# Optimization experiments

Measured on AMD Instinct MI355X. Metric: run time of the kernel, lower is better.

Reference implementation:

```python
import jax, jax.numpy as jnp
import numpy as np
import math

HIDDEN = 1024
HEADS = 16
HEAD = HIDDEN // HEADS
B, N = 2, 2048
NEG_INF = -10000.0


def setup_inputs() -> dict:
    key = jax.random.key(0)
    k1, k2, k3, k4, k5 = jax.random.split(key, 5)
    s = 1.0 / math.sqrt(HIDDEN)
    return {
        "encodings": jax.random.normal(k1, (B, N, HIDDEN), dtype=jnp.float32),
        "attn_w": jax.random.uniform(k2, (3 * HIDDEN, HIDDEN), minval=-s, maxval=s, dtype=jnp.float32),
        "attn_b": jax.random.uniform(k3, (3 * HIDDEN,), minval=-s, maxval=s, dtype=jnp.float32),
        "out_w": jax.random.uniform(k4, (HIDDEN, HIDDEN), minval=-s, maxval=s, dtype=jnp.float32),
        "out_b": jax.random.uniform(k5, (HIDDEN,), minval=-s, maxval=s, dtype=jnp.float32),
    }


def reference(encodings, attn_w, attn_b, out_w, out_b):
    b, n, _ = encodings.shape
    qkv = encodings @ attn_w.T + attn_b                      # [b, n, 3*hidden]
    # 'b n (h l) -> b h n l' with l = 3*head_size
    qkv = qkv.reshape(b, n, HEADS, 3 * HEAD).transpose(0, 2, 1, 3)  # [b, h, n, 3d]
    q, k, v = jnp.split(qkv, 3, axis=-1)                     # each [b, h, n, d]
    # causal mask: key index k attends only if k <= q
    mask = jnp.arange(n)[:, None] <= jnp.arange(n)[None, :]  # [k, q]
    scores = jnp.einsum('bhki,bhqi->bhkq', k, q) / math.sqrt(HEAD)
    scores = jnp.where(mask, scores, NEG_INF)
    probs = jax.nn.softmax(scores, axis=2)                   # softmax over k
    combined = jnp.einsum('bhkq,bhkl->bhql', probs, v)       # [b, h, n, d]
    out = combined.transpose(0, 2, 1, 3).reshape(b, n, HIDDEN)
    return out @ out_w.T + out_b
```

## Files before the change

kernel.cpp:

```cpp
#include <hip/hip_runtime.h>
#include <hip/hip_bf16.h>
#include <stdint.h>

#define HIDDEN 1024
#define NHEADS 16
#define DHEAD  64
#define BATCH  2
#define SEQ    2048
#define MROWS  (BATCH*SEQ)
#define QKVC   (3*HIDDEN)

typedef unsigned short u16;
typedef unsigned int   u32;
typedef __bf16 bf16x8 __attribute__((ext_vector_type(8)));
typedef __bf16 bf16x2 __attribute__((ext_vector_type(2)));
typedef float  f32x4  __attribute__((ext_vector_type(4)));
typedef float  f32x16 __attribute__((ext_vector_type(16)));
typedef short  s16x4  __attribute__((ext_vector_type(4)));
typedef u16    u16x8  __attribute__((ext_vector_type(8)));
typedef u32    u32x2  __attribute__((ext_vector_type(2)));

typedef const __attribute__((address_space(1))) void gvoid_t;
typedef       __attribute__((address_space(3))) void lvoid_t;

__device__ __forceinline__ gvoid_t* to_glob(const void* p){
  return (gvoid_t*)(uintptr_t)p;
}
__device__ __forceinline__ lvoid_t* to_lds(void* p){
  return (lvoid_t*)(uintptr_t)p;
}
__device__ __forceinline__ u32 lds_off(const void* p){
  return (u32)(uintptr_t)p;
}

__device__ __forceinline__ u16 f2bf(float x){
  __bf16 h = (__bf16)x;
  return __builtin_bit_cast(u16, h);
}
__device__ __forceinline__ u32 pk2(float a, float b){
  bf16x2 t = { (__bf16)a, (__bf16)b };
  return __builtin_bit_cast(u32, t);
}

#define MFMA32(a, b, c) __builtin_amdgcn_mfma_f32_32x32x16_bf16(a, b, c, 0, 0, 0)

__global__ __launch_bounds__(256) void k_cvt(const float* __restrict__ in,
                                             u16* __restrict__ out, int n4){
  int i = blockIdx.x * 256 + threadIdx.x;
  if (i >= n4) return;
  const float4 v = reinterpret_cast<const float4*>(in)[i];
  ushort4 o;
  o.x = f2bf(v.x); o.y = f2bf(v.y); o.z = f2bf(v.z); o.w = f2bf(v.w);
  reinterpret_cast<ushort4*>(out)[i] = o;
}

template<int NC, bool BF16OUT>
__global__ __launch_bounds__(256) void k_gemm(const u16* __restrict__ A,
                                              const u16* __restrict__ B,
                                              const float* __restrict__ bias,
                                              void* __restrict__ C){
  constexpr int K = HIDDEN;
  __shared__ u16 As[2][128*32];
  __shared__ u16 Bs[2][128*32];
  const int m0 = blockIdx.x * 128;
  const int n0 = blockIdx.y * 128;
  const int tid = threadIdx.x;
  const int w = tid >> 6, l = tid & 63;
  const int wr = w >> 1, wc = w & 1;

  const f32x4 fz = {0.f, 0.f, 0.f, 0.f};
  f32x4 acc[4][4];
  #pragma unroll
  for (int i = 0; i < 4; ++i)
    #pragma unroll
    for (int j = 0; j < 4; ++j) acc[i][j] = fz;

  const u16* ap = A + (size_t)(m0 + (tid >> 2)) * K + (tid & 3) * 8;
  const u16* bp = B + (size_t)(n0 + (tid >> 2)) * K + (tid & 3) * 8;

  auto stage = [&](int k0, int buf){
    __builtin_amdgcn_global_load_lds(to_glob(ap + k0),        to_lds(&As[buf][w*512]),        16, 0, 0);
    __builtin_amdgcn_global_load_lds(to_glob(ap + 64*K + k0), to_lds(&As[buf][2048 + w*512]), 16, 0, 0);
    __builtin_amdgcn_global_load_lds(to_glob(bp + k0),        to_lds(&Bs[buf][w*512]),        16, 0, 0);
    __builtin_amdgcn_global_load_lds(to_glob(bp + 64*K + k0), to_lds(&Bs[buf][2048 + w*512]), 16, 0, 0);
  };

  stage(0, 0);
  __syncthreads();

  for (int k0 = 0; k0 < K; k0 += 32){
    const int cur = (k0 >> 5) & 1;
    if (k0 + 32 < K) stage(k0 + 32, cur ^ 1);

    bf16x8 af[4], bfr[4];
    #pragma unroll
    for (int mf = 0; mf < 4; ++mf)
      af[mf]  = *(const bf16x8*)&As[cur][(wr*64 + mf*16 + (l & 15))*32 + (l >> 4)*8];
    #pragma unroll
    for (int nf = 0; nf < 4; ++nf)
      bfr[nf] = *(const bf16x8*)&Bs[cur][(wc*64 + nf*16 + (l & 15))*32 + (l >> 4)*8];
    #pragma unroll
    for (int mf = 0; mf < 4; ++mf)
      #pragma unroll
      for (int nf = 0; nf < 4; ++nf)
        acc[mf][nf] = __builtin_amdgcn_mfma_f32_16x16x32_bf16(af[mf], bfr[nf], acc[mf][nf], 0, 0, 0);

    __syncthreads();
  }

  #pragma unroll
  for (int nf = 0; nf < 4; ++nf){
    const int col = n0 + wc*64 + nf*16 + (l & 15);
    const float bv = bias[col];
    #pragma unroll
    for (int mf = 0; mf < 4; ++mf){
      #pragma unroll
      for (int r = 0; r < 4; ++r){
        const int row = m0 + wr*64 + mf*16 + (l >> 4)*4 + r;
        const float v = acc[mf][nf][r] + bv;
        if constexpr (BF16OUT) ((u16*)C)[(size_t)row * NC + col] = f2bf(v);
        else                   ((float*)C)[(size_t)row * NC + col] = v;
      }
    }
  }
}

__global__ __launch_bounds__(256) void k_attn(const u16* __restrict__ qkv,
                                              u16* __restrict__ aout){
  __shared__ u16 smem[2*16384];

  const int bh = blockIdx.x;
  const int b  = bh >> 4;
  const int h  = bh & 15;
  const int qt = 31 - blockIdx.y;
  const int tid = threadIdx.x;
  const int l  = tid & 63;
  const int w  = tid >> 6;
  const int hr = w >> 1;
  const int wr = w & 1;
  const int t128 = tid & 127;
  const int lw = t128 >> 6;
  const int nk = qt + 1;
  const int n0 = nk >> 1;
  const int myn = hr ? (nk - n0) : n0;
  const int kb  = hr ? n0 : 0;
  const int trips = nk - n0;
  const int q0 = qt*64 + wr*32;
  const size_t base = (size_t)b * SEQ * QKVC + (size_t)h * 192;
  const float CEXP = 0.18033688011112042f;

  u16* const Kreg = smem + hr*16384;
  u16* const Vreg = smem + hr*16384 + 8192;

  bf16x8 qf[4];
  {
    const u16* qp = qkv + base + (size_t)(q0 + (l & 31)) * QKVC + (l >> 5) * 8;
    #pragma unroll
    for (int dd = 0; dd < 4; ++dd) qf[dd] = *(const bf16x8*)(qp + dd*16);
  }

  f32x16 o0{}, o1{};
  float m = -1e30f, lsum = 0.f;

  auto stageK = [&](int kt, int cb){
    #pragma unroll
    for (int t = 0; t < 4; ++t){
      const int i  = t*128 + t128;
      const int kr = i >> 3;
      const int cg = (i & 7) ^ (kr & 7);
      const u16* src = qkv + base + (size_t)(kt*64 + kr) * QKVC + 64 + cg * 8;
      __builtin_amdgcn_global_load_lds(to_glob(src), to_lds(&Kreg[cb*4096 + t*1024 + lw*512]), 16, 0, 0);
    }
  };
  auto loadV = [&](int kt, u16x8* vt){
    #pragma unroll
    for (int t = 0; t < 4; ++t){
      const int i = t*128 + t128;
      const int k = i >> 3, d0 = (i & 7) * 8;
      vt[t] = *(const u16x8*)(qkv + base + (size_t)(kt*64 + k) * QKVC + 128 + d0);
    }
  };
  auto writeV = [&](int cb, const u16x8* vt){
    #pragma unroll
    for (int t = 0; t < 4; ++t){
      const int i = t*128 + t128;
      const int k = i >> 3, d0 = (i & 7) * 8;
      const int eo = (k >> 2)*256 + (d0 >> 4)*64 + (k & 3)*16 + (d0 & 15);
      *(u16x8*)&Vreg[cb*4096 + eo] = vt[t];
    }
  };

  if (myn > 0){
    u16x8 vt[4];
    stageK(kb, 0);
    loadV(kb, vt);
    writeV(0, vt);
  }
  __syncthreads();

  const u32 vbase = lds_off(Vreg) + (l & 15)*8 + ((l >> 4) & 1)*128 + (l >> 5)*1024;

  for (int it = 0; it < trips; ++it){
    const int cur = it & 1;
    const bool act = (it < myn);
    const bool pf  = (it + 1 < myn);
    u16x8 vt[4];
    if (pf){ loadV(kb + it + 1, vt); stageK(kb + it + 1, cur ^ 1); }

    if (act){
      const int kt = kb + it;
      f32x16 a0{}, a1{};
      #pragma unroll
      for (int dd = 0; dd < 4; ++dd){
        const int r0 = l & 31, r1 = 32 + (l & 31);
        const int c  = dd*2 + (l >> 5);
        const bf16x8 k0 = *(const bf16x8*)&Kreg[cur*4096 + r0*64 + (c ^ (r0 & 7))*8];
        const bf16x8 k1 = *(const bf16x8*)&Kreg[cur*4096 + r1*64 + (c ^ (r1 & 7))*8];
        a0 = MFMA32(k0, qf[dd], a0);
        a1 = MFMA32(k1, qf[dd], a1);
      }

      if (hr == 1 && it == myn - 1){
        const int qg = q0 + (l & 31);
        #pragma unroll
        for (int r = 0; r < 16; ++r){
          const int kg = kt*64 + (r & 3) + 8*(r >> 2) + 4*(l >> 5);
          if (kg      > qg) a0[r] = -1e30f;
          if (kg + 32 > qg) a1[r] = -1e30f;
        }
      }

      float pm = -1e30f;
      #pragma unroll
      for (int r = 0; r < 16; ++r)
        pm = fmaxf(pm, fmaxf(a0[r], a1[r]));
      pm = fmaxf(pm, __shfl(pm, l ^ 32));

      s16x4 tr[16];
      {
        const u32 vb = vbase + (cur ? 8192u : 0u);
        #pragma unroll
        for (int kk = 0; kk < 4; ++kk){
          asm volatile("ds_read_b64_tr_b16 %0, %4 offset:0\n\t"
                       "ds_read_b64_tr_b16 %1, %4 offset:512\n\t"
                       "ds_read_b64_tr_b16 %2, %4 offset:256\n\t"
                       "ds_read_b64_tr_b16 %3, %4 offset:768"
                       : "=&v"(tr[kk*4+0]), "=&v"(tr[kk*4+1]),
                         "=&v"(tr[kk*4+2]), "=&v"(tr[kk*4+3])
                       : "v"(vb + kk*2048));
        }
      }

      if (__any(pm > m + 64.f)){
        const float mn = fmaxf(m, pm);
        const float corr = exp2f((m - mn) * CEXP);
        m = mn;
        lsum *= corr;
        #pragma unroll
        for (int r = 0; r < 16; ++r){
          const int row = (r & 3) + 8*(r >> 2) + 4*(l >> 5);
          const float cr = __shfl(corr, row | (l & 32));
          o0[r] *= cr; o1[r] *= cr;
        }
      }
      #pragma unroll
      for (int r = 0; r < 16; ++r){
        const float p0 = exp2f((a0[r] - m) * CEXP);
        const float p1 = exp2f((a1[r] - m) * CEXP);
        lsum += p0 + p1;
        a0[r] = p0; a1[r] = p1;
      }

      asm volatile("s_waitcnt lgkmcnt(0)" ::: "memory");
      __builtin_amdgcn_sched_barrier(0);
      #pragma unroll
      for (int kk = 0; kk < 4; ++kk){
        const f32x16& Ac = (kk < 2) ? a0 : a1;
        const int o = (kk & 1) * 8;
        const u32 x0 = pk2(Ac[o+0], Ac[o+1]);
        const u32 x1 = pk2(Ac[o+2], Ac[o+3]);
        const u32 y0 = pk2(Ac[o+4], Ac[o+5]);
        const u32 y1 = pk2(Ac[o+6], Ac[o+7]);
        const u32x2 r0 = __builtin_amdgcn_permlane32_swap(x0, y0, false, false);
        const u32x2 r1 = __builtin_amdgcn_permlane32_swap(x1, y1, false, false);
        union { u32 wd[4]; bf16x8 v; } af;
        af.wd[0] = r0[0]; af.wd[1] = r1[0]; af.wd[2] = r0[1]; af.wd[3] = r1[1];
        union { s16x4 hh[2]; bf16x8 v; } b0, b1;
        b0.hh[0] = tr[kk*4+0]; b0.hh[1] = tr[kk*4+1];
        b1.hh[0] = tr[kk*4+2]; b1.hh[1] = tr[kk*4+3];
        o0 = MFMA32(af.v, b0.v, o0);
        o1 = MFMA32(af.v, b1.v, o1);
      }
    }

    if (pf) writeV(cur ^ 1, vt);
    __syncthreads();
  }

  lsum += __shfl(lsum, l ^ 32);
  float* const Osh  = (float*)smem;
  float2* const MLsh = (float2*)((char*)smem + 16384);

  if (hr == 1){
    #pragma unroll
    for (int r = 0; r < 16; ++r){
      Osh[wr*2048 + l*32 + r]      = o0[r];
      Osh[wr*2048 + l*32 + 16 + r] = o1[r];
    }
    MLsh[wr*64 + l] = float2{m, lsum};
  }
  __syncthreads();

  if (hr == 0){
    const float2 ml1 = MLsh[wr*64 + l];
    const float mm = fmaxf(m, ml1.x);
    const float c0 = exp2f((m - mm) * CEXP);
    const float c1 = exp2f((ml1.x - mm) * CEXP);
    const float lm = lsum*c0 + ml1.y*c1;
    const float a0q = c0 / lm;
    const float a1q = c1 / lm;
    #pragma unroll
    for (int r = 0; r < 16; ++r){
      const int row = (r & 3) + 8*(r >> 2) + 4*(l >> 5);
      const float f0 = __shfl(a0q, row | (l & 32));
      const float f1 = __shfl(a1q, row | (l & 32));
      const int qg = q0 + row;
      u16* op = aout + (size_t)(b*SEQ + qg) * HIDDEN + h*64 + (l & 31);
      op[0]  = f2bf(o0[r]*f0 + Osh[wr*2048 + l*32 + r]*f1);
      op[32] = f2bf(o1[r]*f0 + Osh[wr*2048 + l*32 + 16 + r]*f1);
    }
  }
}

extern "C" void kernel_launch(void* const* d_in, const int* in_sizes, int n_in,
                              void* d_out, int out_size, void* d_ws, size_t ws_size,
                              hipStream_t stream){
  const float* enc    = (const float*)d_in[0];
  const float* attn_w = (const float*)d_in[1];
  const float* attn_b = (const float*)d_in[2];
  const float* out_w  = (const float*)d_in[3];
  const float* out_b  = (const float*)d_in[4];

  char* ws = (char*)d_ws;
  u16* enc_bf = (u16*)(ws);
  u16* wa_bf  = (u16*)(ws + (size_t)( 8u << 20));
  u16* wo_bf  = (u16*)(ws + (size_t)(14u << 20));
  u16* qkv    = (u16*)(ws + (size_t)(16u << 20));
  u16* aout   = enc_bf;

  k_cvt<<<dim3((MROWS*HIDDEN/4 + 255)/256), 256, 0, stream>>>(enc,    enc_bf, MROWS*HIDDEN/4);
  k_cvt<<<dim3((QKVC*HIDDEN/4  + 255)/256), 256, 0, stream>>>(attn_w, wa_bf,  QKVC*HIDDEN/4);
  k_cvt<<<dim3((HIDDEN*HIDDEN/4+ 255)/256), 256, 0, stream>>>(out_w,  wo_bf,  HIDDEN*HIDDEN/4);

  k_gemm<QKVC,  true ><<<dim3(MROWS/128, QKVC/128),  256, 0, stream>>>(enc_bf, wa_bf, attn_b, qkv);
  k_attn<<<dim3(32, 32), 256, 0, stream>>>(qkv, aout);
  k_gemm<HIDDEN, false><<<dim3(MROWS/128, HIDDEN/128), 256, 0, stream>>>(aout, wo_bf, out_b, d_out);
}
```

Measured before the change: 125.9 us.

## Use 32-key tiles with async LDS staging for K and V in attention

The key tile shrinks from 64 to 32 rows, so LDS use halves and the kernel requests four blocks per CU through launch_bounds. V now goes straight into its transposed LDS layout with global_load_lds instead of passing through registers and a separate LDS write, removing that register round-trip. The two half-blocks split the causal key range evenly at 32-key granularity. The trade-off is twice as many loop iterations and __syncthreads barriers, with less MFMA work per iteration to hide latency.

```diff
diff --git a/kernel.cpp b/kernel.cpp
--- a/kernel.cpp
+++ b/kernel.cpp
@@ -125,9 +125,9 @@
   }
 }
 
-__global__ __launch_bounds__(256) void k_attn(const u16* __restrict__ qkv,
-                                              u16* __restrict__ aout){
-  __shared__ u16 smem[2*16384];
+__global__ __launch_bounds__(256, 4) void k_attn(const u16* __restrict__ qkv,
+                                                 u16* __restrict__ aout){
+  __shared__ u16 smem[16384];
 
   const int bh = blockIdx.x;
   const int b  = bh >> 4;
@@ -140,17 +140,32 @@
   const int wr = w & 1;
   const int t128 = tid & 127;
   const int lw = t128 >> 6;
-  const int nk = qt + 1;
-  const int n0 = nk >> 1;
-  const int myn = hr ? (nk - n0) : n0;
-  const int kb  = hr ? n0 : 0;
-  const int trips = nk - n0;
+  const int U  = qt + 1;
+  const int kb = hr ? U : 0;
   const int q0 = qt*64 + wr*32;
   const size_t base = (size_t)b * SEQ * QKVC + (size_t)h * 192;
   const float CEXP = 0.18033688011112042f;
 
-  u16* const Kreg = smem + hr*16384;
-  u16* const Vreg = smem + hr*16384 + 8192;
+  u16* const Kreg = smem + hr*8192;
+  u16* const Vreg = smem + hr*8192 + 4096;
+
+  const int cgK = (t128 & 7) ^ ((t128 >> 3) & 7);
+  const u16* const baseK = qkv + base + (size_t)(t128 >> 3) * QKVC + 64 + cgK * 8;
+  const int vk = ((t128 >> 5) << 2) | ((t128 >> 1) & 3);
+  const int vd = (((t128 >> 3) & 3) << 4) | ((t128 & 1) << 3);
+  const u16* const baseV = qkv + base + (size_t)vk * QKVC + 128 + vd;
+
+  auto stage = [&](int u, int cb){
+    const u16* pk = baseK + (size_t)u * 32 * QKVC;
+    const u16* pv = baseV + (size_t)u * 32 * QKVC;
+    #pragma unroll
+    for (int t = 0; t < 2; ++t){
+      __builtin_amdgcn_global_load_lds(to_glob(pk + t*16*QKVC),
+                                       to_lds(&Kreg[cb*2048 + t*1024 + lw*512]), 16, 0, 0);
+      __builtin_amdgcn_global_load_lds(to_glob(pv + t*16*QKVC),
+                                       to_lds(&Vreg[cb*2048 + t*1024 + lw*512]), 16, 0, 0);
+    }
+  };
 
   bf16x8 qf[4];
   {
@@ -162,138 +177,93 @@
   f32x16 o0{}, o1{};
   float m = -1e30f, lsum = 0.f;
 
-  auto stageK = [&](int kt, int cb){
-    #pragma unroll
-    for (int t = 0; t < 4; ++t){
-      const int i  = t*128 + t128;
-      const int kr = i >> 3;
-      const int cg = (i & 7) ^ (kr & 7);
-      const u16* src = qkv + base + (size_t)(kt*64 + kr) * QKVC + 64 + cg * 8;
-      __builtin_amdgcn_global_load_lds(to_glob(src), to_lds(&Kreg[cb*4096 + t*1024 + lw*512]), 16, 0, 0);
-    }
-  };
-  auto loadV = [&](int kt, u16x8* vt){
-    #pragma unroll
-    for (int t = 0; t < 4; ++t){
-      const int i = t*128 + t128;
-      const int k = i >> 3, d0 = (i & 7) * 8;
-      vt[t] = *(const u16x8*)(qkv + base + (size_t)(kt*64 + k) * QKVC + 128 + d0);
-    }
-  };
-  auto writeV = [&](int cb, const u16x8* vt){
-    #pragma unroll
-    for (int t = 0; t < 4; ++t){
-      const int i = t*128 + t128;
-      const int k = i >> 3, d0 = (i & 7) * 8;
-      const int eo = (k >> 2)*256 + (d0 >> 4)*64 + (k & 3)*16 + (d0 & 15);
-      *(u16x8*)&Vreg[cb*4096 + eo] = vt[t];
-    }
-  };
-
-  if (myn > 0){
-    u16x8 vt[4];
-    stageK(kb, 0);
-    loadV(kb, vt);
-    writeV(0, vt);
-  }
+  stage(kb, 0);
   __syncthreads();
 
   const u32 vbase = lds_off(Vreg) + (l & 15)*8 + ((l >> 4) & 1)*128 + (l >> 5)*1024;
 
-  for (int it = 0; it < trips; ++it){
+  for (int it = 0; it < U; ++it){
     const int cur = it & 1;
-    const bool act = (it < myn);
-    const bool pf  = (it + 1 < myn);
-    u16x8 vt[4];
-    if (pf){ loadV(kb + it + 1, vt); stageK(kb + it + 1, cur ^ 1); }
-
-    if (act){
-      const int kt = kb + it;
-      f32x16 a0{}, a1{};
-      #pragma unroll
-      for (int dd = 0; dd < 4; ++dd){
-        const int r0 = l & 31, r1 = 32 + (l & 31);
-        const int c  = dd*2 + (l >> 5);
-        const bf16x8 k0 = *(const bf16x8*)&Kreg[cur*4096 + r0*64 + (c ^ (r0 & 7))*8];
-        const bf16x8 k1 = *(const bf16x8*)&Kreg[cur*4096 + r1*64 + (c ^ (r1 & 7))*8];
-        a0 = MFMA32(k0, qf[dd], a0);
-        a1 = MFMA32(k1, qf[dd], a1);
+    const int u = kb + it;
+    if (it + 1 < U) stage(kb + it + 1, cur ^ 1);
+
+    f32x16 a0{};
+    const int r0 = l & 31;
+    #pragma unroll
+    for (int dd = 0; dd < 4; ++dd){
+      const int c = dd*2 + (l >> 5);
+      const bf16x8 k0 = *(const bf16x8*)&Kreg[cur*2048 + r0*64 + ((c ^ (r0 & 7)))*8];
+      a0 = MFMA32(k0, qf[dd], a0);
+    }
+
+    if (u*32 + 31 > q0){
+      const int qg = q0 + (l & 31);
+      #pragma unroll
+      for (int r = 0; r < 16; ++r){
+        const int kg = u*32 + (r & 3) + 8*(r >> 2) + 4*(l >> 5);
+        if (kg > qg) a0[r] = -1e30f;
       }
-
-      if (hr == 1 && it == myn - 1){
-        const int qg = q0 + (l & 31);
-        #pragma unroll
-        for (int r = 0; r < 16; ++r){
-          const int kg = kt*64 + (r & 3) + 8*(r >> 2) + 4*(l >> 5);
-          if (kg      > qg) a0[r] = -1e30f;
-          if (kg + 32 > qg) a1[r] = -1e30f;
-        }
+    }
+
+    float pm = -1e30f;
+    #pragma unroll
+    for (int r = 0; r < 16; ++r) pm = fmaxf(pm, a0[r]);
+    pm = fmaxf(pm, __shfl(pm, l ^ 32));
+
+    s16x4 tr[8];
+    {
+      const u32 vb = vbase + (cur ? 4096u : 0u);
+      #pragma unroll
+      for (int kk = 0; kk < 2; ++kk){
+        asm volatile("ds_read_b64_tr_b16 %0, %4 offset:0\n\t"
+                     "ds_read_b64_tr_b16 %1, %4 offset:512\n\t"
+                     "ds_read_b64_tr_b16 %2, %4 offset:256\n\t"
+                     "ds_read_b64_tr_b16 %3, %4 offset:768"
+                     : "=&v"(tr[kk*4+0]), "=&v"(tr[kk*4+1]),
+                       "=&v"(tr[kk*4+2]), "=&v"(tr[kk*4+3])
+                     : "v"(vb + kk*2048));
       }
-
-      float pm = -1e30f;
-      #pragma unroll
-      for (int r = 0; r < 16; ++r)
-        pm = fmaxf(pm, fmaxf(a0[r], a1[r]));
-      pm = fmaxf(pm, __shfl(pm, l ^ 32));
-
-      s16x4 tr[16];
-      {
-        const u32 vb = vbase + (cur ? 8192u : 0u);
-        #pragma unroll
-        for (int kk = 0; kk < 4; ++kk){
-          asm volatile("ds_read_b64_tr_b16 %0, %4 offset:0\n\t"
-                       "ds_read_b64_tr_b16 %1, %4 offset:512\n\t"
-                       "ds_read_b64_tr_b16 %2, %4 offset:256\n\t"
-                       "ds_read_b64_tr_b16 %3, %4 offset:768"
-                       : "=&v"(tr[kk*4+0]), "=&v"(tr[kk*4+1]),
-                         "=&v"(tr[kk*4+2]), "=&v"(tr[kk*4+3])
-                       : "v"(vb + kk*2048));
-        }
+    }
+
+    if (__any(pm > m + 64.f)){
+      const float mn = fmaxf(m, pm);
+      const float corr = exp2f((m - mn) * CEXP);
+      m = mn;
+      lsum *= corr;
+      #pragma unroll
+      for (int r = 0; r < 16; ++r){
+        const int row = (r & 3) + 8*(r >> 2) + 4*(l >> 5);
+        const float cr = __shfl(corr, row | (l & 32));
+        o0[r] *= cr; o1[r] *= cr;
       }
-
-      if (__any(pm > m + 64.f)){
-        const float mn = fmaxf(m, pm);
-        const float corr = exp2f((m - mn) * CEXP);
-        m = mn;
-        lsum *= corr;
-        #pragma unroll
-        for (int r = 0; r < 16; ++r){
-          const int row = (r & 3) + 8*(r >> 2) + 4*(l >> 5);
-          const float cr = __shfl(corr, row | (l & 32));
-          o0[r] *= cr; o1[r] *= cr;
-        }
-      }
-      #pragma unroll
-      for (int r = 0; r < 16; ++r){
-        const float p0 = exp2f((a0[r] - m) * CEXP);
-        const float p1 = exp2f((a1[r] - m) * CEXP);
-        lsum += p0 + p1;
-        a0[r] = p0; a1[r] = p1;
-      }
-
-      asm volatile("s_waitcnt lgkmcnt(0)" ::: "memory");
-      __builtin_amdgcn_sched_barrier(0);
-      #pragma unroll
-      for (int kk = 0; kk < 4; ++kk){
-        const f32x16& Ac = (kk < 2) ? a0 : a1;
-        const int o = (kk & 1) * 8;
-        const u32 x0 = pk2(Ac[o+0], Ac[o+1]);
-        const u32 x1 = pk2(Ac[o+2], Ac[o+3]);
-        const u32 y0 = pk2(Ac[o+4], Ac[o+5]);
-        const u32 y1 = pk2(Ac[o+6], Ac[o+7]);
-        const u32x2 r0 = __builtin_amdgcn_permlane32_swap(x0, y0, false, false);
-        const u32x2 r1 = __builtin_amdgcn_permlane32_swap(x1, y1, false, false);
-        union { u32 wd[4]; bf16x8 v; } af;
-        af.wd[0] = r0[0]; af.wd[1] = r1[0]; af.wd[2] = r0[1]; af.wd[3] = r1[1];
-        union { s16x4 hh[2]; bf16x8 v; } b0, b1;
-        b0.hh[0] = tr[kk*4+0]; b0.hh[1] = tr[kk*4+1];
-        b1.hh[0] = tr[kk*4+2]; b1.hh[1] = tr[kk*4+3];
-        o0 = MFMA32(af.v, b0.v, o0);
-        o1 = MFMA32(af.v, b1.v, o1);
-      }
-    }
-
-    if (pf) writeV(cur ^ 1, vt);
+    }
+    #pragma unroll
+    for (int r = 0; r < 16; ++r){
+      const float p = exp2f((a0[r] - m) * CEXP);
+      lsum += p;
+      a0[r] = p;
+    }
+
+    asm volatile("s_waitcnt lgkmcnt(0)" ::: "memory");
+    __builtin_amdgcn_sched_barrier(0);
+    #pragma unroll
+    for (int kk = 0; kk < 2; ++kk){
+      const int o = kk * 8;
+      const u32 x0 = pk2(a0[o+0], a0[o+1]);
+      const u32 x1 = pk2(a0[o+2], a0[o+3]);
+      const u32 y0 = pk2(a0[o+4], a0[o+5]);
+      const u32 y1 = pk2(a0[o+6], a0[o+7]);
+      const u32x2 r0v = __builtin_amdgcn_permlane32_swap(x0, y0, false, false);
+      const u32x2 r1v = __builtin_amdgcn_permlane32_swap(x1, y1, false, false);
+      union { u32 wd[4]; bf16x8 v; } af;
+      af.wd[0] = r0v[0]; af.wd[1] = r1v[0]; af.wd[2] = r0v[1]; af.wd[3] = r1v[1];
+      union { s16x4 hh[2]; bf16x8 v; } b0, b1;
+      b0.hh[0] = tr[kk*4+0]; b0.hh[1] = tr[kk*4+1];
+      b1.hh[0] = tr[kk*4+2]; b1.hh[1] = tr[kk*4+3];
+      o0 = MFMA32(af.v, b0.v, o0);
+      o1 = MFMA32(af.v, b1.v, o1);
+    }
+
     __syncthreads();
   }
 
```

Result: faster. 111.1 us (-11.8%).
